# Kernel optimization log

Hardware: AMD Instinct MI355X
Metric: run time of the kernel (lower is better)

## Reference

```python
import jax, jax.numpy as jnp
import numpy as np

B, S, E, H = 4, 2048, 1024, 16
D = E // H  # head_dim = 64


def setup_inputs() -> dict:
    key = jax.random.key(0)
    ks = jax.random.split(key, 5)
    return {
        "x": jax.random.normal(ks[0], (B, S, E), dtype=jnp.float32),
        "w_qkv": jax.random.normal(ks[1], (3 * E, E), dtype=jnp.float32) * (E ** -0.5),
        "b_qkv": jax.random.normal(ks[2], (3 * E,), dtype=jnp.float32) * 0.02,
        "w_proj": jax.random.normal(ks[3], (E, E), dtype=jnp.float32) * (E ** -0.5),
        "b_proj": jax.random.normal(ks[4], (E,), dtype=jnp.float32) * 0.02,
    }


def reference(x, w_qkv, b_qkv, w_proj, b_proj):
    # fused QKV projection: [B,S,E] -> [B,S,3E] -> [B,S,3,H,D]
    qkv = (jnp.einsum("bse,fe->bsf", x, w_qkv) + b_qkv).reshape(B, S, 3, H, D)
    q, k, v = qkv[:, :, 0], qkv[:, :, 1], qkv[:, :, 2]  # each [B,S,H,D]
    scale = 1.0 / jnp.sqrt(jnp.asarray(D, dtype=q.dtype))
    scores = jnp.einsum("bqhd,bkhd->bhqk", q, k) * scale  # [B,H,S,S]
    attn = jax.nn.softmax(scores, axis=-1)
    out = jnp.einsum("bhqk,bkhd->bqhd", attn, v).reshape(B, S, E)
    return jnp.einsum("bse,fe->bsf", out, w_proj) + b_proj
```

## Files before the change

### kernel.cpp

```cpp
#include <hip/hip_runtime.h>
#include <cstdint>
#include <cstddef>

#define B_ 4
#define S_ 2048
#define E_ 1024
#define H_ 16
#define D_ 64
#define M_ (B_*S_)
#define NE_ ((size_t)B_*H_*S_*D_)

typedef unsigned int  u32;
typedef unsigned short u16;
typedef __attribute__((ext_vector_type(8))) short bf16x8;
typedef __attribute__((ext_vector_type(4))) float f32x4;
typedef __attribute__((ext_vector_type(2))) unsigned int u32x2;

__device__ __forceinline__ u16 f2bf(float x) {
    u32 u = __float_as_uint(x);
    u32 r = (u + 0x7FFFu + ((u >> 16) & 1u)) >> 16;
    return (u16)r;
}
__device__ __forceinline__ float bf2f(u16 h) { return __uint_as_float((u32)h << 16); }

__device__ __forceinline__ u32 cvtpk_bf16(float lo, float hi) {
    u32 r;
    asm("v_cvt_pk_bf16_f32 %0, %1, %2" : "=v"(r) : "v"(lo), "v"(hi));
    return r;
}

__device__ __forceinline__ void gload_lds16(const void* gsrc, void* lds) {
    __builtin_amdgcn_global_load_lds(
        (const __attribute__((address_space(1))) u32*)gsrc,
        (__attribute__((address_space(3))) u32*)lds, 16, 0, 0);
}


__global__ __launch_bounds__(256)
void convert_img(const float* __restrict__ src, u16* __restrict__ dh, u16* __restrict__ dl)
{
    const int tile = blockIdx.x;
    const int rt = tile >> 5, kt = tile & 31;
    const size_t tb = (size_t)tile * 2048;
    const int ci = threadIdx.x;
    const int l  = ci >> 3;
    const int ph = ci & 7;
    const int s  = ph ^ (l & 7);
    const int r  = (l << 1) | (s >> 2);
    const int k0 = (s & 3) << 3;
    const float* sp = src + ((size_t)(rt * 64 + r)) * 1024 + kt * 32 + k0;
    const float4 f0 = *(const float4*)sp;
    const float4 f1 = *(const float4*)(sp + 4);
    const float vals[8] = {f0.x, f0.y, f0.z, f0.w, f1.x, f1.y, f1.z, f1.w};
    __align__(16) short hs[8];
    __align__(16) short ls[8];
    #pragma unroll
    for (int j = 0; j < 8; ++j) {
        const u16 h = f2bf(vals[j]);
        hs[j] = (short)h;
        ls[j] = (short)f2bf(vals[j] - bf2f(h));
    }
    *(bf16x8*)(dh + tb + ci * 8) = *(const bf16x8*)hs;
    *(bf16x8*)(dl + tb + ci * 8) = *(const bf16x8*)ls;
}

__global__ __launch_bounds__(512, 1)
void gemm_qkv(const u16* __restrict__ AIh, const u16* __restrict__ AIl,
              const u16* __restrict__ BIh, const u16* __restrict__ BIl,
              const float* __restrict__ bias,
              u16* __restrict__ qh, u16* __restrict__ ql,
              u16* __restrict__ kh,
              u16* __restrict__ vh, u16* __restrict__ vl)
{
    __shared__ __align__(16) u16 sT[3][12][2048];

    constexpr int GY = 24;
    constexpr int NCH = (32 * GY) >> 3;

    const int tid = threadIdx.x, lane = tid & 63, w = tid >> 6;
    const int quad = lane >> 4, l15 = lane & 15;

    const int flat = blockIdx.x;
    const int swz  = (flat & 7) * NCH + (flat >> 3);
    const int bx   = swz / GY, by = swz % GY;

    const int m0  = bx * 256;
    const int n0  = by * 128;
    const int mt0 = bx * 4;
    const int nt0 = by * 2;
    const int rw  = w >> 1;
    const int cw  = w & 1;

    const u16* srcq[6];
    #pragma unroll
    for (int it = 0; it < 6; ++it) {
        const int g = w * 6 + it;
        const int t = g >> 2, qtr = g & 3;
        const u16* img = (t < 4) ? AIh : (t < 8) ? AIl : (t < 10) ? BIh : BIl;
        const int rtile = (t < 8) ? (mt0 + (t & 3)) : (nt0 + (t & 1));
        srcq[it] = img + (size_t)rtile * (32 * 2048) + qtr * 512 + lane * 8;
    }

    f32x4 acc[4][4];
    #pragma unroll
    for (int i = 0; i < 4; ++i)
        #pragma unroll
        for (int j = 0; j < 4; ++j)
            acc[i][j] = (f32x4){0.f, 0.f, 0.f, 0.f};

    #pragma unroll
    for (int it = 0; it < 6; ++it)
        gload_lds16(srcq[it], (char*)&sT[0][0][0] + (w * 6 + it) * 1024);
    #pragma unroll
    for (int it = 0; it < 6; ++it)
        gload_lds16(srcq[it] + 2048, (char*)&sT[1][0][0] + (w * 6 + it) * 1024);

    int cb = 0;
    for (int kt = 0; kt < 32; ++kt) {
        if (kt < 31) asm volatile("s_waitcnt vmcnt(6)" ::: "memory");
        else         asm volatile("s_waitcnt vmcnt(0)" ::: "memory");
        asm volatile("s_barrier" ::: "memory");

        if (kt + 2 < 32) {
            int nb = cb + 2; if (nb >= 3) nb -= 3;
            #pragma unroll
            for (int it = 0; it < 6; ++it)
                gload_lds16(srcq[it] + (size_t)(kt + 2) * 2048,
                            (char*)&sT[nb][0][0] + (w * 6 + it) * 1024);
        }

        bf16x8 aH[4], aL[4], bH[4], bL[4];
        #pragma unroll
        for (int i = 0; i < 4; ++i) {
            const int r = i * 16 + l15, l = r >> 1;
            const int off = l * 64 + (((((r & 1) << 2) + quad) ^ (l & 7)) << 3);
            aH[i] = *(const bf16x8*)&sT[cb][rw][off];
            aL[i] = *(const bf16x8*)&sT[cb][4 + rw][off];
        }
        #pragma unroll
        for (int j = 0; j < 4; ++j) {
            const int r = j * 16 + l15, l = r >> 1;
            const int off = l * 64 + (((((r & 1) << 2) + quad) ^ (l & 7)) << 3);
            bH[j] = *(const bf16x8*)&sT[cb][8 + cw][off];
            bL[j] = *(const bf16x8*)&sT[cb][10 + cw][off];
        }

        __builtin_amdgcn_s_setprio(1);
        #pragma unroll
        for (int i = 0; i < 4; ++i)
            #pragma unroll
            for (int j = 0; j < 4; ++j) {
                acc[i][j] = __builtin_amdgcn_mfma_f32_16x16x32_bf16(aL[i], bH[j], acc[i][j], 0, 0, 0);
                acc[i][j] = __builtin_amdgcn_mfma_f32_16x16x32_bf16(aH[i], bL[j], acc[i][j], 0, 0, 0);
                acc[i][j] = __builtin_amdgcn_mfma_f32_16x16x32_bf16(aH[i], bH[j], acc[i][j], 0, 0, 0);
            }
        __builtin_amdgcn_s_setprio(0);

        cb += 1; if (cb >= 3) cb = 0;
    }

    const int fbase = n0 + cw * 64;
    float bj[4];
    #pragma unroll
    for (int j = 0; j < 4; ++j) bj[j] = bias[fbase + j * 16 + l15];

    const int cR = fbase >> 10;
    const int hh = (fbase >> 6) & 15;
    #pragma unroll
    for (int i = 0; i < 4; ++i)
        #pragma unroll
        for (int j = 0; j < 4; ++j)
            #pragma unroll
            for (int reg = 0; reg < 4; ++reg) {
                float val = acc[i][j][reg] + bj[j];
                const int m = m0 + rw * 64 + i * 16 + quad * 4 + reg;
                const int d = j * 16 + l15;
                const int bb = m >> 11, s = m & 2047;
                const int bh = bb * 16 + hh;
                if (cR == 0) val *= 0.18033688011112042f;
                const u16 h = f2bf(val);
                if (cR == 0) {
                    const u16 lo = f2bf(val - bf2f(h));
                    const size_t idx = ((size_t)bh * 2048 + s) * 64 + d;
                    qh[idx] = h; ql[idx] = lo;
                } else if (cR == 1) {
                    const size_t tile = (size_t)bh * 32 + (s >> 6);
                    const int r = s & 63;
                    const size_t off = (tile << 12) + r * 64 + (((d >> 3) ^ (r & 7)) << 3) + (d & 7);
                    kh[off] = h;
                } else {
                    const u16 lo = f2bf(val - bf2f(h));
                    const size_t tile = (size_t)bh * 32 + (s >> 6);
                    const size_t off = (tile << 12) + d * 64 + ((((s & 63) >> 3) ^ (d & 7)) << 3) + (s & 7);
                    vh[off] = h; vl[off] = lo;
                }
            }
}

__global__ __launch_bounds__(512, 2)
void gemm_proj(const u16* __restrict__ AIh, const u16* __restrict__ AIl,
               const u16* __restrict__ BIh, const u16* __restrict__ BIl,
               const float* __restrict__ bias, float* __restrict__ Cout)
{
    __shared__ __align__(16) u16 sT[2][12][2048];

    const int tid = threadIdx.x, lane = tid & 63, w = tid >> 6;
    const int quad = lane >> 4, l15 = lane & 15;
    const int bx = blockIdx.x, by = blockIdx.y;
    const int m0  = bx * 256;
    const int n0  = by * 128;
    const int mt0 = bx * 4;
    const int nt0 = by * 2;
    const int rw  = w >> 1;
    const int cw  = w & 1;

    const u16* srcq[6];
    #pragma unroll
    for (int it = 0; it < 6; ++it) {
        const int g = w * 6 + it;
        const int t = g >> 2, qtr = g & 3;
        const u16* img = (t < 4) ? AIh : (t < 8) ? AIl : (t < 10) ? BIh : BIl;
        const int rtile = (t < 8) ? (mt0 + (t & 3)) : (nt0 + (t & 1));
        srcq[it] = img + (size_t)rtile * (32 * 2048) + qtr * 512 + lane * 8;
    }

    f32x4 acc[4][4];
    #pragma unroll
    for (int i = 0; i < 4; ++i)
        #pragma unroll
        for (int j = 0; j < 4; ++j)
            acc[i][j] = (f32x4){0.f, 0.f, 0.f, 0.f};

    #pragma unroll
    for (int it = 0; it < 6; ++it)
        gload_lds16(srcq[it], (char*)&sT[0][0][0] + (w * 6 + it) * 1024);
    __syncthreads();

    #pragma unroll 2
    for (int kt = 0; kt < 32; ++kt) {
        const int cur = kt & 1;
        bf16x8 aH[4], aL[4], bH[4], bL[4];
        #pragma unroll
        for (int i = 0; i < 4; ++i) {
            const int r = i * 16 + l15, l = r >> 1;
            const int off = l * 64 + (((((r & 1) << 2) + quad) ^ (l & 7)) << 3);
            aH[i] = *(const bf16x8*)&sT[cur][rw][off];
            aL[i] = *(const bf16x8*)&sT[cur][4 + rw][off];
        }
        #pragma unroll
        for (int j = 0; j < 4; ++j) {
            const int r = j * 16 + l15, l = r >> 1;
            const int off = l * 64 + (((((r & 1) << 2) + quad) ^ (l & 7)) << 3);
            bH[j] = *(const bf16x8*)&sT[cur][8 + cw][off];
            bL[j] = *(const bf16x8*)&sT[cur][10 + cw][off];
        }
        if (kt < 31) {
            #pragma unroll
            for (int it = 0; it < 6; ++it)
                gload_lds16(srcq[it] + (size_t)(kt + 1) * 2048,
                            (char*)&sT[cur ^ 1][0][0] + (w * 6 + it) * 1024);
        }
        __builtin_amdgcn_s_setprio(1);
        #pragma unroll
        for (int i = 0; i < 4; ++i)
            #pragma unroll
            for (int j = 0; j < 4; ++j) {
                acc[i][j] = __builtin_amdgcn_mfma_f32_16x16x32_bf16(aL[i], bH[j], acc[i][j], 0, 0, 0);
                acc[i][j] = __builtin_amdgcn_mfma_f32_16x16x32_bf16(aH[i], bL[j], acc[i][j], 0, 0, 0);
                acc[i][j] = __builtin_amdgcn_mfma_f32_16x16x32_bf16(aH[i], bH[j], acc[i][j], 0, 0, 0);
            }
        __builtin_amdgcn_s_setprio(0);
        __syncthreads();
    }

    const int fbase = n0 + cw * 64;
    float bj[4];
    #pragma unroll
    for (int j = 0; j < 4; ++j) bj[j] = bias[fbase + j * 16 + l15];
    #pragma unroll
    for (int i = 0; i < 4; ++i)
        #pragma unroll
        for (int j = 0; j < 4; ++j)
            #pragma unroll
            for (int reg = 0; reg < 4; ++reg) {
                const int m = m0 + rw * 64 + i * 16 + quad * 4 + reg;
                const int f = fbase + j * 16 + l15;
                Cout[(size_t)m * 1024 + f] = acc[i][j][reg] + bj[j];
            }
}

__global__ __launch_bounds__(256, 3)
void attn_mfma(const u16* __restrict__ qh, const u16* __restrict__ ql,
               const u16* __restrict__ kh,
               const u16* __restrict__ vh, const u16* __restrict__ vl,
               u16* __restrict__ oh, u16* __restrict__ ol)
{
    __shared__ __align__(16) u16 KV[3][4096];

    const int tid  = threadIdx.x;
    const int lane = tid & 63, w = tid >> 6;
    const int quad = lane >> 4, l15 = lane & 15;
    const int bh = blockIdx.y;
    const int q0 = blockIdx.x * 128 + w * 32;

    bf16x8 Qf[2][2][2];
    #pragma unroll
    for (int qs = 0; qs < 2; ++qs)
        #pragma unroll
        for (int kk = 0; kk < 2; ++kk) {
            const size_t idx = ((size_t)bh * S_ + q0 + qs * 16 + l15) * 64 + kk * 32 + quad * 8;
            Qf[qs][kk][0] = *(const bf16x8*)(qh + idx);
            Qf[qs][kk][1] = *(const bf16x8*)(ql + idx);
        }

    f32x4 O[2][4];
    float l_part[2] = {0.f, 0.f};
    #pragma unroll
    for (int qs = 0; qs < 2; ++qs)
        #pragma unroll
        for (int ds = 0; ds < 4; ++ds)
            O[qs][ds] = (f32x4){0.f, 0.f, 0.f, 0.f};

    const char* gk[3] = {(const char*)kh, (const char*)vh, (const char*)vl};

    for (int kt = 0; kt < S_ / 64; ++kt) {
        __syncthreads();
        const size_t tb = (((size_t)bh * 32 + kt) << 13);
        #pragma unroll
        for (int a = 0; a < 3; ++a)
            #pragma unroll
            for (int it = 0; it < 2; ++it) {
                const int off = w * 2048 + it * 1024;
                gload_lds16(gk[a] + tb + off + lane * 16, (char*)&KV[a][0] + off);
            }
        __syncthreads();

        f32x4 S[2][4];
        #pragma unroll
        for (int qs = 0; qs < 2; ++qs)
            #pragma unroll
            for (int ks = 0; ks < 4; ++ks)
                S[qs][ks] = (f32x4){-23.083120654223414f, -23.083120654223414f,
                                    -23.083120654223414f, -23.083120654223414f};

        __builtin_amdgcn_s_setprio(1);
        #pragma unroll
        for (int ks = 0; ks < 4; ++ks) {
            const int r = ks * 16 + l15;
            #pragma unroll
            for (int kk = 0; kk < 2; ++kk) {
                const int c = (kk * 4 + quad) ^ (r & 7);
                const bf16x8 Kh = *(const bf16x8*)&KV[0][r * 64 + c * 8];
                #pragma unroll
                for (int qs = 0; qs < 2; ++qs) {
                    S[qs][ks] = __builtin_amdgcn_mfma_f32_16x16x32_bf16(Kh, Qf[qs][kk][1], S[qs][ks], 0, 0, 0);
                    S[qs][ks] = __builtin_amdgcn_mfma_f32_16x16x32_bf16(Kh, Qf[qs][kk][0], S[qs][ks], 0, 0, 0);
                }
            }
        }
        __builtin_amdgcn_s_setprio(0);

        u32 PA[2][2][4];
        #pragma unroll
        for (int qs = 0; qs < 2; ++qs) {
            float lsum = 0.f;
            u32 PK[4][2];
            #pragma unroll
            for (int ks = 0; ks < 4; ++ks) {
                const float p0 = __builtin_exp2f(S[qs][ks][0]);
                const float p1 = __builtin_exp2f(S[qs][ks][1]);
                const float p2 = __builtin_exp2f(S[qs][ks][2]);
                const float p3 = __builtin_exp2f(S[qs][ks][3]);
                lsum += (p0 + p1) + (p2 + p3);
                PK[ks][0] = cvtpk_bf16(p0, p1);
                PK[ks][1] = cvtpk_bf16(p2, p3);
            }
            l_part[qs] += lsum;
            #pragma unroll
            for (int kk = 0; kk < 2; ++kk) {
                const u32x2 t0 = __builtin_amdgcn_permlane32_swap(PK[2 * kk][0], PK[2 * kk + 1][0], false, false);
                const u32x2 w02 = __builtin_amdgcn_permlane16_swap(t0.x, t0.y, false, false);
                const u32x2 t1 = __builtin_amdgcn_permlane32_swap(PK[2 * kk][1], PK[2 * kk + 1][1], false, false);
                const u32x2 w13 = __builtin_amdgcn_permlane16_swap(t1.x, t1.y, false, false);
                PA[qs][kk][0] = w02.x;
                PA[qs][kk][1] = w13.x;
                PA[qs][kk][2] = w02.y;
                PA[qs][kk][3] = w13.y;
            }
        }

        __builtin_amdgcn_s_setprio(1);
        #pragma unroll
        for (int kk = 0; kk < 2; ++kk) {
            union { u32 w4[4]; bf16x8 v; } pu0, pu1;
            #pragma unroll
            for (int c = 0; c < 4; ++c) { pu0.w4[c] = PA[0][kk][c]; pu1.w4[c] = PA[1][kk][c]; }
            const bf16x8 paf[2] = {pu0.v, pu1.v};
            #pragma unroll
            for (int ds = 0; ds < 4; ++ds) {
                const int r = ds * 16 + l15;
                const int c = (kk * 4 + quad) ^ (r & 7);
                const bf16x8 Vh = *(const bf16x8*)&KV[1][r * 64 + c * 8];
                const bf16x8 Vl = *(const bf16x8*)&KV[2][r * 64 + c * 8];
                #pragma unroll
                for (int qs = 0; qs < 2; ++qs) {
                    O[qs][ds] = __builtin_amdgcn_mfma_f32_16x16x32_bf16(Vl, paf[qs], O[qs][ds], 0, 0, 0);
                    O[qs][ds] = __builtin_amdgcn_mfma_f32_16x16x32_bf16(Vh, paf[qs], O[qs][ds], 0, 0, 0);
                }
            }
        }
        __builtin_amdgcn_s_setprio(0);
    }

    float linv[2];
    #pragma unroll
    for (int qs = 0; qs < 2; ++qs) {
        float rs = l_part[qs];
        rs += __shfl_xor(rs, 16);
        rs += __shfl_xor(rs, 32);
        linv[qs] = 1.f / rs;
    }

    const int bb = bh >> 4, hh = bh & 15;
    #pragma unroll
    for (int qs = 0; qs < 2; ++qs) {
        const float inv = linv[qs];
        const int s = q0 + qs * 16 + l15;
        const int m = bb * 2048 + s;
        const int mt = m >> 6, r = m & 63;
        const int l = r >> 1;
        const size_t tb0 = ((size_t)(mt * 32 + hh * 2)) * 2048;
        #pragma unroll
        for (int ds = 0; ds < 4; ++ds) {
            const int d0 = ds * 16 + quad * 4;
            const float v0 = O[qs][ds][0] * inv;
            const float v1 = O[qs][ds][1] * inv;
            const float v2 = O[qs][ds][2] * inv;
            const float v3 = O[qs][ds][3] * inv;
            const u32 h01 = cvtpk_bf16(v0, v1);
            const u32 h23 = cvtpk_bf16(v2, v3);
            const float r0 = v0 - bf2f((u16)h01);
            const float r1 = v1 - bf2f((u16)(h01 >> 16));
            const float r2 = v2 - bf2f((u16)h23);
            const float r3 = v3 - bf2f((u16)(h23 >> 16));
            const u32 l01 = cvtpk_bf16(r0, r1);
            const u32 l23 = cvtpk_bf16(r2, r3);
            const int c  = (d0 & 31) >> 3;
            const int ph = (((r & 1) << 2) + c) ^ (l & 7);
            const size_t off = tb0 + (size_t)(d0 >> 5) * 2048 + l * 64 + ph * 8 + (d0 & 7);
            *(u32x2*)(oh + off) = (u32x2){h01, h23};
            *(u32x2*)(ol + off) = (u32x2){l01, l23};
        }
    }
}

extern "C" void kernel_launch(void* const* d_in, const int* in_sizes, int n_in,
                              void* d_out, int out_size, void* d_ws, size_t ws_size,
                              hipStream_t stream) {
    const float* x      = (const float*)d_in[0];
    const float* w_qkv  = (const float*)d_in[1];
    const float* b_qkv  = (const float*)d_in[2];
    const float* w_proj = (const float*)d_in[3];
    const float* b_proj = (const float*)d_in[4];
    float* out = (float*)d_out;

    u16* qh  = (u16*)d_ws;
    u16* ql  = qh + NE_;
    u16* kh  = ql + NE_;
    u16* vh  = kh + NE_;
    u16* vl  = vh + NE_;
    u16* xh  = vl + NE_;
    u16* xl  = xh + NE_;
    u16* wqh = xl + NE_;
    u16* wql = wqh + (size_t)3 * 1024 * 1024;
    u16* oh  = xh;
    u16* ol  = xl;
    u16* wph = wqh;
    u16* wpl = wph + (size_t)1024 * 1024;

    convert_img<<<128 * 32, 256, 0, stream>>>(x, xh, xl);
    convert_img<<<48 * 32, 256, 0, stream>>>(w_qkv, wqh, wql);

    {
        dim3 grid(32 * 24);
        gemm_qkv<<<grid, 512, 0, stream>>>(xh, xl, wqh, wql,
                                           b_qkv, qh, ql, kh, vh, vl);
    }
    {
        dim3 grid(S_ / 128, B_ * H_);
        attn_mfma<<<grid, 256, 0, stream>>>(qh, ql, kh, vh, vl, oh, ol);
    }
    convert_img<<<16 * 32, 256, 0, stream>>>(w_proj, wph, wpl);
    {
        dim3 grid(M_ / 256, E_ / 128);
        gemm_proj<<<grid, 512, 0, stream>>>(oh, ol, wph, wpl, b_proj, out);
    }
}
```

Measured before the change: 443.3 us.

## Shrink QKV GEMM to 128x128 tiles with 256-thread double-buffered pipeline

The QKV projection GEMM moves from 256x128 tiles on 512 threads with a triple-buffered LDS pipeline and an XCD-aware block swizzle to 128x128 tiles on 256 threads with two blocks per CU. It now double-buffers with a full __syncthreads each k-step and uses a plain 2D grid with no swizzle. The aim is higher occupancy and a smaller LDS footprint per block. The trade-off is less operand reuse per tile, a shallower prefetch distance, an extra barrier per iteration, and losing the L2-locality swizzle.

```diff
diff --git a/kernel.cpp b/kernel.cpp
--- a/kernel.cpp
+++ b/kernel.cpp
@@ -64,7 +64,7 @@
     *(bf16x8*)(dl + tb + ci * 8) = *(const bf16x8*)ls;
 }
 
-__global__ __launch_bounds__(512, 1)
+__global__ __launch_bounds__(256, 2)
 void gemm_qkv(const u16* __restrict__ AIh, const u16* __restrict__ AIl,
               const u16* __restrict__ BIh, const u16* __restrict__ BIl,
               const float* __restrict__ bias,
@@ -72,32 +72,25 @@
               u16* __restrict__ kh,
               u16* __restrict__ vh, u16* __restrict__ vl)
 {
-    __shared__ __align__(16) u16 sT[3][12][2048];
-
-    constexpr int GY = 24;
-    constexpr int NCH = (32 * GY) >> 3;
+    __shared__ __align__(16) u16 sT[2][8][2048];
 
     const int tid = threadIdx.x, lane = tid & 63, w = tid >> 6;
     const int quad = lane >> 4, l15 = lane & 15;
-
-    const int flat = blockIdx.x;
-    const int swz  = (flat & 7) * NCH + (flat >> 3);
-    const int bx   = swz / GY, by = swz % GY;
-
-    const int m0  = bx * 256;
+    const int bx = blockIdx.x, by = blockIdx.y;
+    const int m0  = bx * 128;
     const int n0  = by * 128;
-    const int mt0 = bx * 4;
+    const int mt0 = bx * 2;
     const int nt0 = by * 2;
     const int rw  = w >> 1;
     const int cw  = w & 1;
 
-    const u16* srcq[6];
-    #pragma unroll
-    for (int it = 0; it < 6; ++it) {
-        const int g = w * 6 + it;
+    const u16* srcq[8];
+    #pragma unroll
+    for (int it = 0; it < 8; ++it) {
+        const int g = w * 8 + it;
         const int t = g >> 2, qtr = g & 3;
-        const u16* img = (t < 4) ? AIh : (t < 8) ? AIl : (t < 10) ? BIh : BIl;
-        const int rtile = (t < 8) ? (mt0 + (t & 3)) : (nt0 + (t & 1));
+        const u16* img = (t < 2) ? AIh : (t < 4) ? AIl : (t < 6) ? BIh : BIl;
+        const int rtile = ((t < 4) ? mt0 : nt0) + (t & 1);
         srcq[it] = img + (size_t)rtile * (32 * 2048) + qtr * 512 + lane * 8;
     }
 
@@ -109,42 +102,34 @@
             acc[i][j] = (f32x4){0.f, 0.f, 0.f, 0.f};
 
     #pragma unroll
-    for (int it = 0; it < 6; ++it)
-        gload_lds16(srcq[it], (char*)&sT[0][0][0] + (w * 6 + it) * 1024);
-    #pragma unroll
-    for (int it = 0; it < 6; ++it)
-        gload_lds16(srcq[it] + 2048, (char*)&sT[1][0][0] + (w * 6 + it) * 1024);
-
-    int cb = 0;
+    for (int it = 0; it < 8; ++it)
+        gload_lds16(srcq[it], (char*)&sT[0][0][0] + (w * 8 + it) * 1024);
+    __syncthreads();
+
+    #pragma unroll 2
     for (int kt = 0; kt < 32; ++kt) {
-        if (kt < 31) asm volatile("s_waitcnt vmcnt(6)" ::: "memory");
-        else         asm volatile("s_waitcnt vmcnt(0)" ::: "memory");
-        asm volatile("s_barrier" ::: "memory");
-
-        if (kt + 2 < 32) {
-            int nb = cb + 2; if (nb >= 3) nb -= 3;
-            #pragma unroll
-            for (int it = 0; it < 6; ++it)
-                gload_lds16(srcq[it] + (size_t)(kt + 2) * 2048,
-                            (char*)&sT[nb][0][0] + (w * 6 + it) * 1024);
-        }
-
+        const int cur = kt & 1;
+        if (kt < 31) {
+            #pragma unroll
+            for (int it = 0; it < 8; ++it)
+                gload_lds16(srcq[it] + (size_t)(kt + 1) * 2048,
+                            (char*)&sT[cur ^ 1][0][0] + (w * 8 + it) * 1024);
+        }
         bf16x8 aH[4], aL[4], bH[4], bL[4];
         #pragma unroll
         for (int i = 0; i < 4; ++i) {
             const int r = i * 16 + l15, l = r >> 1;
             const int off = l * 64 + (((((r & 1) << 2) + quad) ^ (l & 7)) << 3);
-            aH[i] = *(const bf16x8*)&sT[cb][rw][off];
-            aL[i] = *(const bf16x8*)&sT[cb][4 + rw][off];
+            aH[i] = *(const bf16x8*)&sT[cur][rw][off];
+            aL[i] = *(const bf16x8*)&sT[cur][2 + rw][off];
         }
         #pragma unroll
         for (int j = 0; j < 4; ++j) {
             const int r = j * 16 + l15, l = r >> 1;
             const int off = l * 64 + (((((r & 1) << 2) + quad) ^ (l & 7)) << 3);
-            bH[j] = *(const bf16x8*)&sT[cb][8 + cw][off];
-            bL[j] = *(const bf16x8*)&sT[cb][10 + cw][off];
-        }
-
+            bH[j] = *(const bf16x8*)&sT[cur][4 + cw][off];
+            bL[j] = *(const bf16x8*)&sT[cur][6 + cw][off];
+        }
         __builtin_amdgcn_s_setprio(1);
         #pragma unroll
         for (int i = 0; i < 4; ++i)
@@ -155,8 +140,7 @@
                 acc[i][j] = __builtin_amdgcn_mfma_f32_16x16x32_bf16(aH[i], bH[j], acc[i][j], 0, 0, 0);
             }
         __builtin_amdgcn_s_setprio(0);
-
-        cb += 1; if (cb >= 3) cb = 0;
+        __syncthreads();
     }
 
     const int fbase = n0 + cw * 64;
@@ -482,8 +466,8 @@
     convert_img<<<48 * 32, 256, 0, stream>>>(w_qkv, wqh, wql);
 
     {
-        dim3 grid(32 * 24);
-        gemm_qkv<<<grid, 512, 0, stream>>>(xh, xl, wqh, wql,
+        dim3 grid(M_ / 128, (3 * E_) / 128);
+        gemm_qkv<<<grid, 256, 0, stream>>>(xh, xl, wqh, wql,
                                            b_qkv, qh, ql, kh, vh, vl);
     }
     {
```

Result: faster. 427.8 us (-3.5%).
